# Kernel optimization log

Measured on AMD Instinct MI355X. Metric: run time of the kernel, lower is better.

The kernel has to match this reference:

```python
import jax, jax.numpy as jnp
import numpy as np

B, T, C, L = 32, 800, 5000, 100  # batch, frames, vocab(incl blank=0), max label len
NEG = -1e30  # log-zero surrogate (safe for logsumexp, avoids inf-inf NaNs)


def setup_inputs() -> dict:
    key = jax.random.key(0)
    k1, k2_, k3, k4 = jax.random.split(key, 4)
    # nnet_output is assumed to be log-softmax output of the acoustic model
    nnet_output = jax.nn.log_softmax(jax.random.normal(k1, (B, T, C), jnp.float32), axis=-1)
    targets = jax.random.randint(k2_, (B, L), 1, C).astype(jnp.int32)  # labels in [1, C)
    input_lengths = (T - jax.random.randint(k3, (B,), 0, T // 4)).astype(jnp.int32)
    target_lengths = (L - jax.random.randint(k4, (B,), 0, L // 4)).astype(jnp.int32)
    return dict(nnet_output=nnet_output, targets=targets,
                input_lengths=input_lengths, target_lengths=target_lengths)


def _ctc_tot_scores(log_probs, targets, input_lengths, target_lengths):
    """Log-semiring total score of the CTC numerator lattice per utterance.
    Equivalent to k2.intersect_dense(num_graphs, dense_fsa_vec).get_tot_scores(log_semiring=True).
    """
    Bb, Tt, Cc = log_probs.shape
    Ll = targets.shape[1]
    S = 2 * Ll + 1  # extended label sequence with interleaved blanks
    ext = jnp.zeros((Bb, S), targets.dtype).at[:, 1::2].set(targets)  # [B,S]
    # emission scores gathered along the extended labels: [B,T,S]
    emit = jnp.take_along_axis(log_probs, jnp.broadcast_to(ext[:, None, :], (Bb, Tt, S)), axis=2)
    emit_seq = jnp.transpose(emit, (1, 0, 2))  # [T,B,S]
    # skip transition s-2 -> s allowed iff ext[s] != blank and ext[s] != ext[s-2]
    ext_m2 = jnp.pad(ext[:, :-2], ((0, 0), (2, 0)), constant_values=-1)
    skip_ok = (ext != 0) & (ext != ext_m2)  # [B,S]

    alpha0 = jnp.full((Bb, S), NEG, log_probs.dtype)
    alpha0 = alpha0.at[:, 0].set(emit_seq[0, :, 0]).at[:, 1].set(emit_seq[0, :, 1])

    def step(alpha, emit_t):
        a1 = alpha
        a2 = jnp.pad(alpha[:, :-1], ((0, 0), (1, 0)), constant_values=NEG)
        a3 = jnp.where(skip_ok, jnp.pad(alpha[:, :-2], ((0, 0), (2, 0)), constant_values=NEG), NEG)
        m = jnp.maximum(jnp.maximum(a1, a2), a3)
        new = m + jnp.log(jnp.exp(a1 - m) + jnp.exp(a2 - m) + jnp.exp(a3 - m)) + emit_t
        return new, new

    _, alphas_rest = jax.lax.scan(step, alpha0, emit_seq[1:])
    alphas = jnp.concatenate([alpha0[None], alphas_rest], axis=0)  # [T,B,S]

    bidx = jnp.arange(Bb)
    final_alpha = alphas[input_lengths - 1, bidx, :]  # [B,S] alpha at last valid frame
    s_last = 2 * target_lengths       # final blank state
    s_prev = 2 * target_lengths - 1   # final label state
    tot = jnp.logaddexp(final_alpha[bidx, s_last], final_alpha[bidx, s_prev])  # [B]
    return tot


def reference(nnet_output, targets, input_lengths, target_lengths):
    tot_scores = _ctc_tot_scores(nnet_output, targets, input_lengths, target_lengths)
    finite = tot_scores > (NEG / 2)  # mirrors get_tot_objf_and_num_frames filtering -inf
    frames = input_lengths.astype(jnp.int64)
    tot_score = jnp.sum(jnp.where(finite, tot_scores, 0.0))
    tot_frames = jnp.sum(jnp.where(finite, frames, 0))
    all_frames = jnp.sum(frames)
    return (tot_score, tot_frames, all_frames)
```

## Files before the change

kernel.cpp:

```cpp
#include <hip/hip_runtime.h>


constexpr int B = 32;
constexpr int T = 800;
constexpr int C = 5000;
constexpr int L = 100;
constexpr int S = 2 * L + 1;
constexpr int SP = 204;
constexpr float NEGV = -1e30f;

__global__ __launch_bounds__(256) void gather_emit(
    const float* __restrict__ lp, const int* __restrict__ targets,
    const int* __restrict__ il, float* __restrict__ emit)
{
    const int t = blockIdx.x;
    const int b = blockIdx.y;
    if (t >= il[b]) return;
    const int s = threadIdx.x;
    if (s >= S) return;
    const int cls = (s & 1) ? targets[b * L + (s >> 1)] : 0;
    const size_t row = (size_t)(b * T + t);
    emit[row * SP + s] = lp[row * C + cls];
}

__global__ __launch_bounds__(64) void ctc_alpha(
    const float* __restrict__ emit, const int* __restrict__ targets,
    const int* __restrict__ il_, const int* __restrict__ tl_,
    float* __restrict__ out)
{
    const int b    = blockIdx.x;
    const int lane = threadIdx.x;
    const int il   = il_[b];
    const int tl   = tl_[b];
    const float* erow = emit + (size_t)b * T * SP;
    const int s0 = lane * 4;

    bool skip[4];
#pragma unroll
    for (int j = 0; j < 4; ++j) {
        const int s = s0 + j;
        bool sk = false;
        if ((s & 1) && s < S) {
            const int cur  = targets[b * L + (s >> 1)];
            const int prev = (s >= 3) ? targets[b * L + (s >> 1) - 1] : -1;
            sk = (cur != prev);
        }
        skip[j] = sk;
    }

    float4 e0 = make_float4(NEGV, NEGV, NEGV, NEGV);
    if (s0 < S) e0 = *(const float4*)(erow + s0);
    float a[4];
    a[0] = (s0 == 0) ? e0.x : NEGV;
    a[1] = (s0 == 0) ? e0.y : NEGV;
    a[2] = NEGV;
    a[3] = NEGV;

    float4 pref = make_float4(NEGV, NEGV, NEGV, NEGV);
    if (il > 1 && s0 < S) pref = *(const float4*)(erow + (size_t)SP + s0);

    for (int t = 1; t < il; ++t) {
        const float4 e = pref;
        const int tn = (t + 1 < il) ? (t + 1) : t;
        if (s0 < S) pref = *(const float4*)(erow + (size_t)SP * tn + s0);

        float up_a3 = __shfl_up(a[3], 1);
        float up_a2 = __shfl_up(a[2], 1);
        if (lane == 0) { up_a3 = NEGV; up_a2 = NEGV; }

        const float em[4]   = { e.x, e.y, e.z, e.w };
        const float a2in[4] = { up_a3, a[0], a[1], a[2] };
        const float a3in[4] = { up_a2, up_a3, a[0], a[1] };
        float na[4];
#pragma unroll
        for (int j = 0; j < 4; ++j) {
            const float a1 = a[j];
            const float a2 = a2in[j];
            const float a3 = skip[j] ? a3in[j] : NEGV;
            const float m  = fmaxf(a1, fmaxf(a2, a3));
            const float sum = __expf(a1 - m) + __expf(a2 - m) + __expf(a3 - m);
            na[j] = m + __logf(sum) + em[j];
        }
        a[0] = na[0]; a[1] = na[1]; a[2] = na[2]; a[3] = na[3];
    }

    __shared__ float sm[256];
    sm[s0 + 0] = a[0];
    sm[s0 + 1] = a[1];
    sm[s0 + 2] = a[2];
    sm[s0 + 3] = a[3];
    __syncthreads();

    if (lane == 0) {
        const float va = sm[2 * tl];
        const float vb = sm[2 * tl - 1];
        const float m  = fmaxf(va, vb);
        const float tot = m + __logf(__expf(va - m) + __expf(vb - m));
        const bool finite = tot > (NEGV * 0.5f);
        atomicAdd(out + 0, finite ? tot : 0.0f);
        atomicAdd(out + 1, finite ? (float)il : 0.0f);
        atomicAdd(out + 2, (float)il);
    }
}

extern "C" void kernel_launch(void* const* d_in, const int* in_sizes, int n_in,
                              void* d_out, int out_size, void* d_ws, size_t ws_size,
                              hipStream_t stream)
{
    const float* lp      = (const float*)d_in[0];
    const int*   targets = (const int*)d_in[1];
    const int*   il      = (const int*)d_in[2];
    const int*   tl      = (const int*)d_in[3];
    float* out  = (float*)d_out;
    float* emit = (float*)d_ws;

    hipMemsetAsync(d_out, 0, (size_t)out_size * sizeof(float), stream);

    dim3 g1(T, B);
    gather_emit<<<g1, 256, 0, stream>>>(lp, targets, il, emit);
    ctc_alpha<<<B, 64, 0, stream>>>(emit, targets, il, tl, out);
}
```

Measured before the change: 831.2 us.

## Fuse emission gather into CTC alpha recursion with register prefetch ring

Drops the separate gather kernel and the intermediate emission buffer. The recursion kernel now reads the blank and label log-probs directly from the input, keeping a prefetch ring PF frames deep in registers. It also skips the exp for the third term where no skip transition is allowed. The cost is scattered reads from the large input inside the serial loop, which the prefetch depth has to cover.

```diff
diff --git a/kernel.cpp b/kernel.cpp
--- a/kernel.cpp
+++ b/kernel.cpp
@@ -6,25 +6,20 @@
 constexpr int C = 5000;
 constexpr int L = 100;
 constexpr int S = 2 * L + 1;
-constexpr int SP = 204;
+constexpr int PF = 8;
 constexpr float NEGV = -1e30f;
 
-__global__ __launch_bounds__(256) void gather_emit(
-    const float* __restrict__ lp, const int* __restrict__ targets,
-    const int* __restrict__ il, float* __restrict__ emit)
-{
-    const int t = blockIdx.x;
-    const int b = blockIdx.y;
-    if (t >= il[b]) return;
-    const int s = threadIdx.x;
-    if (s >= S) return;
-    const int cls = (s & 1) ? targets[b * L + (s >> 1)] : 0;
-    const size_t row = (size_t)(b * T + t);
-    emit[row * SP + s] = lp[row * C + cls];
+__device__ __forceinline__ float lse2(float a, float b) {
+    const float m = fmaxf(a, b);
+    return m + __logf(__expf(a - m) + __expf(b - m));
+}
+__device__ __forceinline__ float lse3(float a, float b, float c) {
+    const float m = fmaxf(a, fmaxf(b, c));
+    return m + __logf(__expf(a - m) + __expf(b - m) + __expf(c - m));
 }
 
-__global__ __launch_bounds__(64) void ctc_alpha(
-    const float* __restrict__ emit, const int* __restrict__ targets,
+__global__ __launch_bounds__(64) void ctc_fused(
+    const float* __restrict__ lp, const int* __restrict__ targets,
     const int* __restrict__ il_, const int* __restrict__ tl_,
     float* __restrict__ out)
 {
@@ -32,70 +27,79 @@
     const int lane = threadIdx.x;
     const int il   = il_[b];
     const int tl   = tl_[b];
-    const float* erow = emit + (size_t)b * T * SP;
-    const int s0 = lane * 4;
 
-    bool skip[4];
-#pragma unroll
-    for (int j = 0; j < 4; ++j) {
-        const int s = s0 + j;
-        bool sk = false;
-        if ((s & 1) && s < S) {
-            const int cur  = targets[b * L + (s >> 1)];
-            const int prev = (s >= 3) ? targets[b * L + (s >> 1) - 1] : -1;
-            sk = (cur != prev);
-        }
-        skip[j] = sk;
+    const int l2 = 2 * lane;
+    const int i1 = (l2     < L) ? l2     : L - 1;
+    const int i3 = (l2 + 1 < L) ? l2 + 1 : L - 1;
+    const int ip = (l2 - 1 >= 0) ? l2 - 1 : 0;
+    const int tb = b * L;
+    const int c1 = targets[tb + i1];
+    const int c3 = targets[tb + i3];
+    const int cp = targets[tb + ip];
+    const bool skip1 = (lane == 0) ? true : (c1 != cp);
+    const bool skip3 = (c3 != c1);
+
+    const float* __restrict__ base = lp + (size_t)b * T * C;
+
+    float a0, a1v, a2v, a3v;
+    {
+        const float bl0 = base[0];
+        const float e01 = base[c1];
+        a0  = (lane == 0) ? bl0 : NEGV;
+        a1v = (lane == 0) ? e01 : NEGV;
+        a2v = NEGV;
+        a3v = NEGV;
     }
 
-    float4 e0 = make_float4(NEGV, NEGV, NEGV, NEGV);
-    if (s0 < S) e0 = *(const float4*)(erow + s0);
-    float a[4];
-    a[0] = (s0 == 0) ? e0.x : NEGV;
-    a[1] = (s0 == 0) ? e0.y : NEGV;
-    a[2] = NEGV;
-    a[3] = NEGV;
+    float rb[PF], r1[PF], r3[PF];
+#pragma unroll
+    for (int k = 0; k < PF; ++k) {
+        int t0 = 1 + k; if (t0 >= il) t0 = il - 1; if (t0 < 0) t0 = 0;
+        const float* rowp = base + (size_t)t0 * C;
+        rb[k] = rowp[0];
+        r1[k] = rowp[c1];
+        r3[k] = rowp[c3];
+    }
 
-    float4 pref = make_float4(NEGV, NEGV, NEGV, NEGV);
-    if (il > 1 && s0 < S) pref = *(const float4*)(erow + (size_t)SP + s0);
+    int t = 1;
+    while (t < il) {
+#pragma unroll
+        for (int k = 0; k < PF; ++k) {
+            if (t < il) {
+                const float bl = rb[k], e1 = r1[k], e3 = r3[k];
 
-    for (int t = 1; t < il; ++t) {
-        const float4 e = pref;
-        const int tn = (t + 1 < il) ? (t + 1) : t;
-        if (s0 < S) pref = *(const float4*)(erow + (size_t)SP * tn + s0);
+                int tn = t + PF; if (tn >= il) tn = il - 1;
+                const float* rowp = base + (size_t)tn * C;
+                rb[k] = rowp[0];
+                r1[k] = rowp[c1];
+                r3[k] = rowp[c3];
 
-        float up_a3 = __shfl_up(a[3], 1);
-        float up_a2 = __shfl_up(a[2], 1);
-        if (lane == 0) { up_a3 = NEGV; up_a2 = NEGV; }
+                float up3 = __shfl_up(a3v, 1);
+                float up2 = __shfl_up(a2v, 1);
+                if (lane == 0) { up3 = NEGV; up2 = NEGV; }
 
-        const float em[4]   = { e.x, e.y, e.z, e.w };
-        const float a2in[4] = { up_a3, a[0], a[1], a[2] };
-        const float a3in[4] = { up_a2, up_a3, a[0], a[1] };
-        float na[4];
-#pragma unroll
-        for (int j = 0; j < 4; ++j) {
-            const float a1 = a[j];
-            const float a2 = a2in[j];
-            const float a3 = skip[j] ? a3in[j] : NEGV;
-            const float m  = fmaxf(a1, fmaxf(a2, a3));
-            const float sum = __expf(a1 - m) + __expf(a2 - m) + __expf(a3 - m);
-            na[j] = m + __logf(sum) + em[j];
+                const float n0 = lse2(a0, up3) + bl;
+                const float n1 = (skip1 ? lse3(a1v, a0, up3) : lse2(a1v, a0)) + e1;
+                const float n2 = lse2(a2v, a1v) + bl;
+                const float n3 = (skip3 ? lse3(a3v, a2v, a1v) : lse2(a3v, a2v)) + e3;
+
+                a0 = n0; a1v = n1; a2v = n2; a3v = n3;
+            }
+            ++t;
         }
-        a[0] = na[0]; a[1] = na[1]; a[2] = na[2]; a[3] = na[3];
     }
 
     __shared__ float sm[256];
-    sm[s0 + 0] = a[0];
-    sm[s0 + 1] = a[1];
-    sm[s0 + 2] = a[2];
-    sm[s0 + 3] = a[3];
+    sm[4 * lane + 0] = a0;
+    sm[4 * lane + 1] = a1v;
+    sm[4 * lane + 2] = a2v;
+    sm[4 * lane + 3] = a3v;
     __syncthreads();
 
     if (lane == 0) {
-        const float va = sm[2 * tl];
-        const float vb = sm[2 * tl - 1];
-        const float m  = fmaxf(va, vb);
-        const float tot = m + __logf(__expf(va - m) + __expf(vb - m));
+        const float va  = sm[2 * tl];
+        const float vb  = sm[2 * tl - 1];
+        const float tot = lse2(va, vb);
         const bool finite = tot > (NEGV * 0.5f);
         atomicAdd(out + 0, finite ? tot : 0.0f);
         atomicAdd(out + 1, finite ? (float)il : 0.0f);
@@ -111,12 +115,8 @@
     const int*   targets = (const int*)d_in[1];
     const int*   il      = (const int*)d_in[2];
     const int*   tl      = (const int*)d_in[3];
-    float* out  = (float*)d_out;
-    float* emit = (float*)d_ws;
+    float* out = (float*)d_out;
 
     hipMemsetAsync(d_out, 0, (size_t)out_size * sizeof(float), stream);
-
-    dim3 g1(T, B);
-    gather_emit<<<g1, 256, 0, stream>>>(lp, targets, il, emit);
-    ctc_alpha<<<B, 64, 0, stream>>>(emit, targets, il, tl, out);
+    ctc_fused<<<B, 64, 0, stream>>>(lp, targets, il, tl, out);
 }
```

Measured after the change: 1.071 ms. 1.29x slower.
